# Optimization experiments

Hardware: AMD Instinct MI355X
Metric: run time of the kernel (lower is better)

The kernel has to match this reference:

```python
import jax, jax.numpy as jnp
import numpy as np
from functools import partial

STRIDES = (8, 16, 32)
SIZES = ((80, 80), (40, 40), (20, 20))
NUM_CLASSES = 80
NMS_THR = 0.65
SCORE_THR = 0.01
MAX_DET = 100  # fixed-size NMS output (padded; validity = scores > 0)


def setup_inputs() -> dict:
    key = jax.random.key(0)
    ks = jax.random.split(key, 9)
    B = 32
    out = {}
    for i, (h, w) in enumerate(SIZES):
        out[f"cls{i}"] = jax.random.normal(ks[3 * i], (B, NUM_CLASSES, h, w), jnp.float32)
        out[f"reg{i}"] = jax.random.normal(ks[3 * i + 1], (B, 4, h, w), jnp.float32)
        out[f"obj{i}"] = jax.random.normal(ks[3 * i + 2], (B, 1, h, w), jnp.float32)
    return out


def _grid_points():
    # MlvlPointGenerator.grid_priors(with_stride=True), offset=0: (x, y, stride, stride)
    pts = []
    for (h, w), s in zip(SIZES, STRIDES):
        xs = jnp.arange(w, dtype=jnp.float32) * s
        ys = jnp.arange(h, dtype=jnp.float32) * s
        xx, yy = jnp.meshgrid(xs, ys)  # [h, w], x varies fastest -> matches NHWC flatten
        st = jnp.full((h * w,), float(s), jnp.float32)
        pts.append(jnp.stack([xx.ravel(), yy.ravel(), st, st], axis=-1))
    return jnp.concatenate(pts, axis=0)  # [A, 4]


def _flatten(t, c):
    # [N, C, H, W] -> [N, H*W, C]  (permute(0,2,3,1).reshape)
    return t.transpose(0, 2, 3, 1).reshape(t.shape[0], -1, c)


def _decode(points, reg):
    # YOLOXBBoxDecoder: center = pred_xy * stride + point, wh = exp(pred_wh) * stride
    stride = points[:, 2:]                       # [A, 2]
    xys = reg[..., :2] * stride + points[:, :2]  # [B, A, 2]
    whs = jnp.exp(reg[..., 2:]) * stride         # [B, A, 2]
    return jnp.concatenate([xys - whs * 0.5, xys + whs * 0.5], axis=-1)  # x1y1x2y2


def _iou_one_vs_all(b, boxes):
    # b: [4], boxes: [A, 4]
    tl = jnp.maximum(b[:2], boxes[:, :2])
    br = jnp.minimum(b[2:], boxes[:, 2:])
    wh = jnp.clip(br - tl, 0.0)
    inter = wh[:, 0] * wh[:, 1]
    a1 = (b[2] - b[0]) * (b[3] - b[1])
    a2 = (boxes[:, 2] - boxes[:, 0]) * (boxes[:, 3] - boxes[:, 1])
    return inter / (a1 + a2 - inter + 1e-6)


def _nms_image(boxes, cls_scores, objectness):
    # boxes [A,4], cls_scores [A,C] (post-sigmoid), objectness [A] (post-sigmoid)
    max_scores = jnp.max(cls_scores, axis=1)
    labels = jnp.argmax(cls_scores, axis=1)
    scores = max_scores * objectness
    live = jnp.where(scores >= SCORE_THR, scores, -jnp.inf)  # score_thr filter

    # batched_nms: offset boxes per class so boxes of different labels never overlap
    offset = jax.lax.stop_gradient(jnp.max(jnp.abs(boxes)) + 1.0)
    boxes_off = jax.lax.stop_gradient(boxes) + labels.astype(boxes.dtype)[:, None] * offset

    def body(i, state):
        live, keep, kscores = state
        best = jnp.argmax(live)
        kscores = kscores.at[i].set(live[best])
        keep = keep.at[i].set(best)
        iou = _iou_one_vs_all(boxes_off[best], boxes_off)
        live = jnp.where(iou > NMS_THR, -jnp.inf, live)
        live = live.at[best].set(-jnp.inf)
        return live, keep, kscores

    keep0 = jnp.zeros((MAX_DET,), jnp.int32)
    ks0 = jnp.full((MAX_DET,), -jnp.inf, boxes.dtype)
    _, keep, kscores = jax.lax.fori_loop(0, MAX_DET, body, (live, keep0, ks0))

    valid = kscores > -jnp.inf
    out_boxes = jnp.where(valid[:, None], boxes[keep], 0.0)
    out_scores = jnp.where(valid, scores[keep], 0.0)
    out_labels = jnp.where(valid, labels[keep], -1)
    return out_boxes, out_scores, out_labels, valid


def _forward(cls0, cls1, cls2, reg0, reg1, reg2, obj0, obj1, obj2):
    B = cls0.shape[0]
    flat_cls = jax.nn.sigmoid(jnp.concatenate([_flatten(c, NUM_CLASSES) for c in (cls0, cls1, cls2)], axis=1))
    flat_reg = jnp.concatenate([_flatten(r, 4) for r in (reg0, reg1, reg2)], axis=1)
    flat_obj = jax.nn.sigmoid(jnp.concatenate([_flatten(o, 1) for o in (obj0, obj1, obj2)], axis=1))[..., 0]
    points = _grid_points()
    boxes = _decode(points, flat_reg)  # [B, A, 4]
    return jax.vmap(_nms_image)(boxes, flat_cls, flat_obj)


@jax.jit
def reference(cls0, cls1, cls2, reg0, reg1, reg2, obj0, obj1, obj2):
    return _forward(cls0, cls1, cls2, reg0, reg1, reg2, obj0, obj1, obj2)
```

## Files before the change

kernel.cpp:

```cpp
#include <hip/hip_runtime.h>
#include <cmath>

typedef unsigned int uint;
typedef unsigned long long ull;

#define BATCH 32
#define NA 8400
#define NC 80
#define MAXDET 100
#define NMSTHR 0.65f
#define SCTHR 0.01f

#define NT 1024
#define NW (NT / 64)
#define EPT 9
#define NBINS 4096
#define CAP 512
#define WTGT 256u

#define DGROUPS 132

__device__ __forceinline__ float stable_sigmoid(float x) {
    if (x >= 0.f) return 1.f / (1.f + expf(-x));
    float e = expf(x);
    return e / (1.f + e);
}

template<int HW, int W, int S>
__device__ __forceinline__ void decode_blk(
    const float* __restrict__ cls, const float* __restrict__ reg,
    const float* __restrict__ obj, int b, int p0, int w, int lane, int ag0,
    float (*s_m)[64], int (*s_c)[64],
    float4* __restrict__ wboxes, int* __restrict__ wlabels, uint* __restrict__ wkeys)
{
    int p = p0 + lane;
    bool valid = (p < HW);
    int pc = valid ? p : (HW - 1);

    const float* cbase = cls + (size_t)b * NC * HW + (size_t)(w * 20) * HW + pc;
    float v[20];
    #pragma unroll
    for (int i = 0; i < 20; ++i) v[i] = cbase[(size_t)i * HW];
    float m = v[0]; int c = 0;
    #pragma unroll
    for (int i = 1; i < 20; ++i)
        if (v[i] > m) { m = v[i]; c = i; }

    s_m[w][lane] = m;
    s_c[w][lane] = c + w * 20;
    __syncthreads();

    if (w == 0) {
        float mm = s_m[0][lane]; int cc = s_c[0][lane];
        #pragma unroll
        for (int ww = 1; ww < 4; ++ww) {
            float om = s_m[ww][lane]; int oc = s_c[ww][lane];
            if (om > mm) { mm = om; cc = oc; }
        }
        const float* rb = reg + (size_t)b * 4 * HW + pc;
        float r0 = rb[0];
        float r1 = rb[HW];
        float r2 = rb[2 * (size_t)HW];
        float r3 = rb[3 * (size_t)HW];
        float ov = obj[(size_t)b * HW + pc];

        int y = pc / W;
        int x = pc - y * W;
        float sc = stable_sigmoid(mm) * stable_sigmoid(ov);
        float cx = r0 * (float)S + (float)x * (float)S;
        float cy = r1 * (float)S + (float)y * (float)S;
        float bw = expf(r2) * (float)S;
        float bh = expf(r3) * (float)S;

        if (valid) {
            int ag = ag0 + lane;
            wboxes[ag]  = make_float4(cx - bw * 0.5f, cy - bh * 0.5f,
                                      cx + bw * 0.5f, cy + bh * 0.5f);
            wlabels[ag] = cc;
            wkeys[ag]   = (sc >= SCTHR) ? ~__float_as_uint(sc) : 0xFFFFFFFFu;
        }
    }
}

__global__ __launch_bounds__(256) void decode_kernel(
    const float* __restrict__ cls0, const float* __restrict__ reg0, const float* __restrict__ obj0,
    const float* __restrict__ cls1, const float* __restrict__ reg1, const float* __restrict__ obj1,
    const float* __restrict__ cls2, const float* __restrict__ reg2, const float* __restrict__ obj2,
    float4* __restrict__ wboxes, int* __restrict__ wlabels, uint* __restrict__ wkeys)
{
    __shared__ float s_m[4][64];
    __shared__ int   s_c[4][64];

    int bid  = blockIdx.x;
    int b    = bid / DGROUPS;
    int g    = bid - b * DGROUPS;
    int t    = threadIdx.x;
    int w    = t >> 6;
    int lane = t & 63;

    if (g < 100) {
        int p0 = g * 64;
        decode_blk<6400, 80, 8>(cls0, reg0, obj0, b, p0, w, lane,
                                b * NA + p0, s_m, s_c, wboxes, wlabels, wkeys);
    } else if (g < 125) {
        int p0 = (g - 100) * 64;
        decode_blk<1600, 40, 16>(cls1, reg1, obj1, b, p0, w, lane,
                                 b * NA + 6400 + p0, s_m, s_c, wboxes, wlabels, wkeys);
    } else {
        int p0 = (g - 125) * 64;
        decode_blk<400, 20, 32>(cls2, reg2, obj2, b, p0, w, lane,
                                b * NA + 8000 + p0, s_m, s_c, wboxes, wlabels, wkeys);
    }
}

__global__ __launch_bounds__(NT) void nms_kernel(
    const float4* __restrict__ wboxes, const int* __restrict__ wlabels,
    const uint* __restrict__ wkeys, float* __restrict__ out)
{
    int b = blockIdx.x;
    int t = threadIdx.x;
    int lane = t & 63;
    int wv = t >> 6;
    const float4* boxes  = wboxes  + (size_t)b * NA;
    const int*    labels = wlabels + (size_t)b * NA;
    const uint*   keys   = wkeys   + (size_t)b * NA;

    __shared__ uint   s_hist[NBINS];
    __shared__ uint   s_cum[NBINS + 1];
    __shared__ uint   s_wsum[NW];
    __shared__ ull    s_skey[CAP];
    __shared__ float4 s_cbox[CAP];
    __shared__ float  s_ca[CAP];
    __shared__ int    s_clb[CAP];
    __shared__ float  s_kbox[MAXDET][4];
    __shared__ float  s_ka1[MAXDET];
    __shared__ int    s_kidx[MAXDET];
    __shared__ float  s_kscr[MAXDET];
    __shared__ int    s_klab[MAXDET];
    __shared__ float  s_red[NW];
    __shared__ float  s_off;
    __shared__ int    s_kept, s_winlo, s_winhi, s_nsel;

    for (int i = t; i < NBINS; i += NT) s_hist[i] = 0;
    if (t == 0) { s_kept = 0; s_winlo = 0; }
    __syncthreads();
    float m = 0.f;
    uint kreg[EPT];
    #pragma unroll
    for (int w = 0; w < EPT; ++w) {
        int e = t + w * NT;
        kreg[w] = 0xFFFFFFFFu;
        if (e < NA) {
            float4 v = boxes[e];
            m = fmaxf(m, fmaxf(fmaxf(fabsf(v.x), fabsf(v.y)),
                               fmaxf(fabsf(v.z), fabsf(v.w))));
            uint k = keys[e];
            kreg[w] = k;
            if (k != 0xFFFFFFFFu) atomicAdd(&s_hist[k >> 20], 1u);
        }
    }
    #pragma unroll
    for (int o = 32; o >= 1; o >>= 1) m = fmaxf(m, __shfl_xor(m, o));
    if (lane == 0) s_red[wv] = m;
    __syncthreads();
    if (t == 0) {
        float mm = 0.f;
        for (int w = 0; w < NW; ++w) mm = fmaxf(mm, s_red[w]);
        s_off = mm + 1.f;
    }

    uint l0 = s_hist[4 * t], l1 = s_hist[4 * t + 1],
         l2 = s_hist[4 * t + 2], l3 = s_hist[4 * t + 3];
    uint L = l0 + l1 + l2 + l3;
    uint ls = L;
    #pragma unroll
    for (int o = 1; o < 64; o <<= 1) {
        uint v = __shfl_up(ls, o);
        if (lane >= o) ls += v;
    }
    if (lane == 63) s_wsum[wv] = ls;
    __syncthreads();
    if (t < NW) {
        uint v = s_wsum[t];
        uint vs = v;
        #pragma unroll
        for (int o = 1; o < NW; o <<= 1) {
            uint u = __shfl_up(vs, o);
            if ((t & 63) >= o) vs += u;
        }
        s_wsum[t] = vs - v;
    }
    __syncthreads();
    uint base = s_wsum[wv] + (ls - L);
    s_cum[4 * t]     = base;
    s_cum[4 * t + 1] = base + l0;
    s_cum[4 * t + 2] = base + l0 + l1;
    s_cum[4 * t + 3] = base + l0 + l1 + l2;
    if (t == NT - 1) s_cum[NBINS] = base + L;
    float off;

    for (;;) {
        __syncthreads();
        int kept = s_kept, winlo = s_winlo;
        uint remaining = s_cum[NBINS] - s_cum[winlo];
        if (kept >= MAXDET || winlo >= NBINS || remaining == 0u) break;
        if (t == 0) { s_winhi = winlo + 1; s_nsel = 0; }
        if (t < CAP) s_skey[t] = ~0ull;
        __syncthreads();
        uint cl = s_cum[winlo];
        #pragma unroll
        for (int q = 0; q < 4; ++q) {
            int i = t + q * NT;
            if (i >= winlo && i < NBINS) {
                bool p0 = (s_cum[i + 1] - cl) <= WTGT;
                bool p1 = (i + 1 < NBINS) && ((s_cum[i + 2] - cl) <= WTGT);
                if (p0 && !p1) s_winhi = i + 1;
            }
        }
        __syncthreads();
        int winhi = s_winhi;

        #pragma unroll
        for (int w = 0; w < EPT; ++w) {
            int e = t + w * NT;
            uint k = kreg[w];
            bool q = false;
            if (k != 0xFFFFFFFFu) {
                int bin = (int)(k >> 20);
                q = (bin >= winlo && bin < winhi);
            }
            ull mask = __ballot(q);
            if (mask) {
                int leader = __ffsll(mask) - 1;
                int pbase = 0;
                if (lane == leader) pbase = atomicAdd(&s_nsel, __popcll(mask));
                pbase = __shfl(pbase, leader);
                if (q) {
                    int pos = pbase + __popcll(mask & ((1ull << lane) - 1ull));
                    if (pos < CAP) s_skey[pos] = ((ull)k << 32) | (uint)e;
                }
            }
        }
        __syncthreads();
        int nsel = s_nsel; if (nsel > CAP) nsel = CAP;

        ull myk = (t < nsel) ? s_skey[t] : ~0ull;
        int rank = 0;
        if (t < nsel) {
            for (int j = 0; j < nsel; ++j)
                rank += (s_skey[j] < myk) ? 1 : 0;
        }
        __syncthreads();
        if (t < nsel) s_skey[rank] = myk;
        __syncthreads();

        off = s_off;
        if (t < nsel) {
            ull sk = s_skey[t];
            if (sk != ~0ull) {
                int idx = (int)(sk & 0xFFFFFFFFull);
                float4 rb = boxes[idx];
                int lb = labels[idx];
                float lo = (float)lb * off;
                float c0 = rb.x + lo, c1 = rb.y + lo;
                float c2 = rb.z + lo, c3 = rb.w + lo;
                s_cbox[t] = make_float4(c0, c1, c2, c3);
                s_ca[t]   = (c2 - c0) * (c3 - c1);
                s_clb[t]  = lb;
            }
        }
        __syncthreads();

        if (t < 64) {
            int kept2 = s_kept;
            for (int cb = 0; cb < nsel && kept2 < MAXDET; cb += 64) {
                int ci = cb + lane;
                ull sk = (ci < nsel) ? s_skey[ci] : ~0ull;
                bool has = (sk != ~0ull);
                int idx = 0, lab = 0;
                float sc = 0.f, c0 = 0.f, c1 = 0.f, c2 = 0.f, c3 = 0.f, ca = 0.f;
                if (has) {
                    idx = (int)(sk & 0xFFFFFFFFull);
                    sc  = __uint_as_float(~(uint)(sk >> 32));
                    float4 cbx = s_cbox[ci];
                    c0 = cbx.x; c1 = cbx.y; c2 = cbx.z; c3 = cbx.w;
                    ca = s_ca[ci];
                    lab = s_clb[ci];
                    for (int q = 0; q < kept2; ++q) {
                        float tlx = fmaxf(s_kbox[q][0], c0);
                        float tly = fmaxf(s_kbox[q][1], c1);
                        float brx = fminf(s_kbox[q][2], c2);
                        float bry = fminf(s_kbox[q][3], c3);
                        float ww = fmaxf(brx - tlx, 0.f);
                        float hh = fmaxf(bry - tly, 0.f);
                        float inter = ww * hh;
                        float iou = inter / (s_ka1[q] + ca - inter + 1e-6f);
                        if (iou > NMSTHR) { has = false; break; }
                    }
                }
                ull am = __ballot(has);
                while (am && kept2 < MAXDET) {
                    int f = __ffsll(am) - 1;
                    float f0 = __shfl(c0, f), f1 = __shfl(c1, f);
                    float f2 = __shfl(c2, f), f3 = __shfl(c3, f);
                    float fa = __shfl(ca, f);
                    if (lane == f) {
                        s_kbox[kept2][0] = c0; s_kbox[kept2][1] = c1;
                        s_kbox[kept2][2] = c2; s_kbox[kept2][3] = c3;
                        s_ka1[kept2] = ca; s_kidx[kept2] = idx;
                        s_kscr[kept2] = sc; s_klab[kept2] = lab;
                        has = false;
                    }
                    kept2++;
                    if (has) {
                        float tlx = fmaxf(f0, c0), tly = fmaxf(f1, c1);
                        float brx = fminf(f2, c2), bry = fminf(f3, c3);
                        float ww = fmaxf(brx - tlx, 0.f), hh = fmaxf(bry - tly, 0.f);
                        float inter = ww * hh;
                        float iou = inter / (fa + ca - inter + 1e-6f);
                        if (iou > NMSTHR) has = false;
                    }
                    am = __ballot(has);
                }
            }
            if (lane == 0) s_kept = kept2;
        }
        __syncthreads();
        if (t == 0) s_winlo = s_winhi;
    }
    __syncthreads();

    if (t < MAXDET) {
        int kept = s_kept;
        float4 obx = make_float4(0.f, 0.f, 0.f, 0.f);
        float osc = 0.f, olab = -1.f, oval = 0.f;
        if (t < kept) {
            int idx = s_kidx[t];
            obx  = boxes[idx];
            osc  = s_kscr[t];
            olab = (float)s_klab[t];
            oval = 1.f;
        }
        float* ob = out + ((size_t)b * MAXDET + t) * 4;
        ob[0] = obx.x; ob[1] = obx.y; ob[2] = obx.z; ob[3] = obx.w;
        out[BATCH * MAXDET * 4 + b * MAXDET + t] = osc;
        out[BATCH * MAXDET * 5 + b * MAXDET + t] = olab;
        out[BATCH * MAXDET * 6 + b * MAXDET + t] = oval;
    }
}

extern "C" void kernel_launch(void* const* d_in, const int* in_sizes, int n_in,
                              void* d_out, int out_size, void* d_ws, size_t ws_size,
                              hipStream_t stream) {
    const float* cls0 = (const float*)d_in[0];
    const float* reg0 = (const float*)d_in[1];
    const float* obj0 = (const float*)d_in[2];
    const float* cls1 = (const float*)d_in[3];
    const float* reg1 = (const float*)d_in[4];
    const float* obj1 = (const float*)d_in[5];
    const float* cls2 = (const float*)d_in[6];
    const float* reg2 = (const float*)d_in[7];
    const float* obj2 = (const float*)d_in[8];

    char* ws = (char*)d_ws;
    size_t nBA = (size_t)BATCH * NA;
    float4* wboxes  = (float4*)ws;
    int*    wlabels = (int*)(ws + nBA * 16);
    uint*   wkeys   = (uint*)(ws + nBA * 20);

    decode_kernel<<<BATCH * DGROUPS, 256, 0, stream>>>(
        cls0, reg0, obj0, cls1, reg1, obj1, cls2, reg2, obj2,
        wboxes, wlabels, wkeys);

    nms_kernel<<<BATCH, NT, 0, stream>>>(wboxes, wlabels, wkeys, (float*)d_out);
}
```

Baseline: 161.0 us.

## Halve NMS block size to 512 threads and fuse rank scatter with box gather

```diff
diff --git a/kernel.cpp b/kernel.cpp
--- a/kernel.cpp
+++ b/kernel.cpp
@@ -11,9 +11,9 @@
 #define NMSTHR 0.65f
 #define SCTHR 0.01f
 
-#define NT 1024
+#define NT 512
 #define NW (NT / 64)
-#define EPT 9
+#define EPT 17
 #define NBINS 4096
 #define CAP 512
 #define WTGT 256u
@@ -169,9 +169,10 @@
         s_off = mm + 1.f;
     }
 
-    uint l0 = s_hist[4 * t], l1 = s_hist[4 * t + 1],
-         l2 = s_hist[4 * t + 2], l3 = s_hist[4 * t + 3];
-    uint L = l0 + l1 + l2 + l3;
+    uint l[8];
+    uint L = 0;
+    #pragma unroll
+    for (int i = 0; i < 8; ++i) { l[i] = s_hist[8 * t + i]; L += l[i]; }
     uint ls = L;
     #pragma unroll
     for (int o = 1; o < 64; o <<= 1) {
@@ -186,17 +187,17 @@
         #pragma unroll
         for (int o = 1; o < NW; o <<= 1) {
             uint u = __shfl_up(vs, o);
-            if ((t & 63) >= o) vs += u;
+            if (t >= o) vs += u;
         }
         s_wsum[t] = vs - v;
     }
     __syncthreads();
-    uint base = s_wsum[wv] + (ls - L);
-    s_cum[4 * t]     = base;
-    s_cum[4 * t + 1] = base + l0;
-    s_cum[4 * t + 2] = base + l0 + l1;
-    s_cum[4 * t + 3] = base + l0 + l1 + l2;
-    if (t == NT - 1) s_cum[NBINS] = base + L;
+    {
+        uint run = s_wsum[wv] + (ls - L);
+        #pragma unroll
+        for (int i = 0; i < 8; ++i) { s_cum[8 * t + i] = run; run += l[i]; }
+        if (t == NT - 1) s_cum[NBINS] = run;
+    }
     float off;
 
     for (;;) {
@@ -205,11 +206,11 @@
         uint remaining = s_cum[NBINS] - s_cum[winlo];
         if (kept >= MAXDET || winlo >= NBINS || remaining == 0u) break;
         if (t == 0) { s_winhi = winlo + 1; s_nsel = 0; }
-        if (t < CAP) s_skey[t] = ~0ull;
+        s_skey[t] = ~0ull;
         __syncthreads();
         uint cl = s_cum[winlo];
         #pragma unroll
-        for (int q = 0; q < 4; ++q) {
+        for (int q = 0; q < 8; ++q) {
             int i = t + q * NT;
             if (i >= winlo && i < NBINS) {
                 bool p0 = (s_cum[i + 1] - cl) <= WTGT;
@@ -244,6 +245,7 @@
         __syncthreads();
         int nsel = s_nsel; if (nsel > CAP) nsel = CAP;
 
+        off = s_off;
         ull myk = (t < nsel) ? s_skey[t] : ~0ull;
         int rank = 0;
         if (t < nsel) {
@@ -251,23 +253,17 @@
                 rank += (s_skey[j] < myk) ? 1 : 0;
         }
         __syncthreads();
-        if (t < nsel) s_skey[rank] = myk;
-        __syncthreads();
-
-        off = s_off;
         if (t < nsel) {
-            ull sk = s_skey[t];
-            if (sk != ~0ull) {
-                int idx = (int)(sk & 0xFFFFFFFFull);
-                float4 rb = boxes[idx];
-                int lb = labels[idx];
-                float lo = (float)lb * off;
-                float c0 = rb.x + lo, c1 = rb.y + lo;
-                float c2 = rb.z + lo, c3 = rb.w + lo;
-                s_cbox[t] = make_float4(c0, c1, c2, c3);
-                s_ca[t]   = (c2 - c0) * (c3 - c1);
-                s_clb[t]  = lb;
-            }
+            s_skey[rank] = myk;
+            int idx = (int)(myk & 0xFFFFFFFFull);
+            float4 rb = boxes[idx];
+            int lb = labels[idx];
+            float lo = (float)lb * off;
+            float c0 = rb.x + lo, c1 = rb.y + lo;
+            float c2 = rb.z + lo, c3 = rb.w + lo;
+            s_cbox[rank] = make_float4(c0, c1, c2, c3);
+            s_ca[rank]   = (c2 - c0) * (c3 - c1);
+            s_clb[rank]  = lb;
         }
         __syncthreads();
 
```

Measured after the change: 164.3 us. 1.02x slower.
